# Kernel optimization log

Measured on AMD Instinct MI355X. Metric: run time of the kernel, lower is better.

The kernel has to match this reference:

```python
import jax, jax.numpy as jnp
import numpy as np

D_MODEL = 768
D_STATE = 16
D_CONV = 4
EXPAND = 2
N_LAYERS = 2
HEADDIM = 64
PATCH_DIM = 256
D_INNER = EXPAND * D_MODEL            # 1536
NHEADS = D_INNER // HEADDIM           # 24
CONV_DIM = D_INNER + 2 * D_STATE      # 1568 (x, B, C share the conv)
D_IN_PROJ = 2 * D_INNER + 2 * D_STATE + NHEADS  # 3128


def _mamba2(u, w_in, conv_w, conv_b, dt_bias, A_log, D, norm_w, w_out):
    """Mamba2 block (ngroups=1, rmsnorm=True, non-fused reference path)."""
    b, l, _ = u.shape
    zxbcdt = u @ w_in                                   # (b,l,D_IN_PROJ)
    z = zxbcdt[..., :D_INNER]
    xBC = zxbcdt[..., D_INNER:D_INNER + CONV_DIM]
    dt = jax.nn.softplus(zxbcdt[..., D_INNER + CONV_DIM:] + dt_bias)  # (b,l,H)
    # causal depthwise conv1d over L, then silu
    kernel = conv_w.T[:, None, :]                       # (D_CONV,1,CONV_DIM)
    xBC = jax.lax.conv_general_dilated(
        xBC, kernel, (1,), [(D_CONV - 1, 0)],
        dimension_numbers=('NLC', 'LIO', 'NLC'),
        feature_group_count=CONV_DIM) + conv_b
    xBC = jax.nn.silu(xBC)
    x = xBC[..., :D_INNER].reshape(b, l, NHEADS, HEADDIM)
    B = xBC[..., D_INNER:D_INNER + D_STATE]             # (b,l,N)
    C = xBC[..., D_INNER + D_STATE:]                    # (b,l,N)
    A = -jnp.exp(A_log)                                 # (H,)

    def step(h, inp):
        dt_t, x_t, b_t, c_t = inp                       # (b,H),(b,H,P),(b,N),(b,N)
        dA = jnp.exp(dt_t * A)                          # (b,H)
        h = h * dA[:, :, None, None] + jnp.einsum('bh,bhp,bn->bhpn', dt_t, x_t, b_t)
        y_t = jnp.einsum('bhpn,bn->bhp', h, c_t)
        return h, y_t

    h0 = jnp.zeros((b, NHEADS, HEADDIM, D_STATE), u.dtype)
    _, y = jax.lax.scan(step, h0,
                        (dt.swapaxes(0, 1), x.swapaxes(0, 1),
                         B.swapaxes(0, 1), C.swapaxes(0, 1)))
    y = y.swapaxes(0, 1) + x * D[:, None]               # skip: D per head
    y = y.reshape(b, l, D_INNER)
    # gated RMSNorm: rmsnorm(y * silu(z)) * weight
    g = y * jax.nn.silu(z)
    g = g * jax.lax.rsqrt(jnp.mean(g * g, axis=-1, keepdims=True) + 1e-5)
    y = g * norm_w
    return y @ w_out


def _backbone(patch_embeddings, Wp, bp, in_w, conv_w, conv_b, dt_bias,
              A_log, Dh, norm_w, out_w, bi_w, ls, fin_w):
    x = patch_embeddings @ Wp + bp
    for i in range(N_LAYERS):
        h_f = _mamba2(x, in_w[i, 0], conv_w[i, 0], conv_b[i, 0], dt_bias[i, 0],
                      A_log[i, 0], Dh[i, 0], norm_w[i, 0], out_w[i, 0])
        h_b = jnp.flip(_mamba2(jnp.flip(x, 1), in_w[i, 1], conv_w[i, 1],
                               conv_b[i, 1], dt_bias[i, 1], A_log[i, 1],
                               Dh[i, 1], norm_w[i, 1], out_w[i, 1]), 1)
        m = jnp.concatenate([h_f, h_b], axis=-1) @ bi_w[i]
        x = x + m * ls[i]
    # final RMSNorm with unit offset
    v = jnp.mean(x * x, axis=-1, keepdims=True)
    return x * jax.lax.rsqrt(v + 1e-6) * (1.0 + fin_w)


def setup_inputs() -> dict:
    key = jax.random.key(0)
    ks = jax.random.split(key, 14)
    L2 = (N_LAYERS, 2)
    pe = jax.random.normal(ks[0], (2, 2048, PATCH_DIM), jnp.float32)
    Wp = jax.random.normal(ks[1], (PATCH_DIM, D_MODEL), jnp.float32) * 0.02
    bp = jnp.zeros((D_MODEL,), jnp.float32)
    in_w = jax.random.normal(ks[2], L2 + (D_MODEL, D_IN_PROJ), jnp.float32) * 0.02
    conv_w = jax.random.normal(ks[3], L2 + (CONV_DIM, D_CONV), jnp.float32) * 0.2
    conv_b = jnp.zeros(L2 + (CONV_DIM,), jnp.float32)
    dt_bias = jax.random.uniform(ks[4], L2 + (NHEADS,), jnp.float32, -4.0, -2.0)
    A_log = jnp.log(jax.random.uniform(ks[5], L2 + (NHEADS,), jnp.float32, 1.0, 16.0))
    Dh = jax.random.normal(ks[6], L2 + (NHEADS,), jnp.float32) * 0.1 + 1.0
    norm_w = jnp.ones(L2 + (D_INNER,), jnp.float32)
    out_w = jax.random.normal(ks[7], L2 + (D_INNER, D_MODEL), jnp.float32) * 0.02
    bi_w = jax.random.normal(ks[8], (N_LAYERS, 2 * D_MODEL, D_MODEL), jnp.float32) * 0.02
    ls = jnp.full((N_LAYERS, D_MODEL), 1e-4, jnp.float32)
    fin_w = jnp.zeros((D_MODEL,), jnp.float32)
    return {"patch_embeddings": pe, "Wp": Wp, "bp": bp, "in_w": in_w,
            "conv_w": conv_w, "conv_b": conv_b, "dt_bias": dt_bias,
            "A_log": A_log, "Dh": Dh, "norm_w": norm_w, "out_w": out_w,
            "bi_w": bi_w, "ls": ls, "fin_w": fin_w}


def reference(patch_embeddings, Wp, bp, in_w, conv_w, conv_b, dt_bias,
              A_log, Dh, norm_w, out_w, bi_w, ls, fin_w):
    return _backbone(patch_embeddings, Wp, bp, in_w, conv_w, conv_b, dt_bias,
                     A_log, Dh, norm_w, out_w, bi_w, ls, fin_w)
```

## Files before the change

### kernel.cpp

```cpp
#include <hip/hip_runtime.h>

typedef unsigned short u16;
typedef short s16x8 __attribute__((ext_vector_type(8)));
typedef u16 u16x8 __attribute__((ext_vector_type(8)));
typedef float f32x4 __attribute__((ext_vector_type(4)));

__device__ inline float bf2f(u16 u) {
    union { unsigned int i; float f; } w; w.i = ((unsigned int)u) << 16; return w.f;
}
__device__ inline u16 f2bf(float f) {
    union { float f; unsigned int i; } w; w.f = f;
    unsigned int u = w.i;
    u += 0x7fffu + ((u >> 16) & 1u);
    return (u16)(u >> 16);
}

__global__ __launch_bounds__(256)
void wtransT(const float* __restrict__ src, u16* __restrict__ dst,
             int K, int N, int dstride, int src_z, int dz_hi, int dz_lo)
{
    int z = blockIdx.z;
    src += (size_t)z * src_z;
    dst += (size_t)(z >> 1) * dz_hi + (size_t)(z & 1) * dz_lo;
    __shared__ float t[32][33];
    int kt = blockIdx.y * 32, nt0 = blockIdx.x * 32;
    int lx = threadIdx.x & 31, ly = threadIdx.x >> 5;
#pragma unroll
    for (int i = 0; i < 32; i += 8) {
        int k = kt + ly + i, n = nt0 + lx;
        t[ly + i][lx] = (k < K && n < N) ? src[(size_t)k * N + n] : 0.f;
    }
    __syncthreads();
#pragma unroll
    for (int i = 0; i < 32; i += 8) {
        int n = nt0 + ly + i, k = kt + lx;
        if (n < N && k < K) dst[(size_t)n * dstride + k] = f2bf(t[lx][ly + i]);
    }
}

__global__ void cvtk(const float* __restrict__ src, u16* __restrict__ dst, int n) {
    int i = blockIdx.x * 256 + threadIdx.x;
    if (i < n) dst[i] = f2bf(src[i]);
}

__global__ __launch_bounds__(256, 2)
void gemm8(const u16* __restrict__ A, const u16* __restrict__ WT,
           int M, int N, int K,
           u16* __restrict__ bout, int ostride)
{
    __shared__ u16 lds8[2 * 16384];

    int mt, nt;
    {
        int nwg = gridDim.x * gridDim.y;
        int f = blockIdx.y * gridDim.x + blockIdx.x;
        int q = nwg >> 3, r = nwg & 7;
        int xcd = f & 7, lo = f >> 3;
        int wid = (xcd < r ? xcd * (q + 1) : r * (q + 1) + (xcd - r) * q) + lo;
        mt = wid % gridDim.y; nt = wid / gridDim.y;
    }

    const int tid  = threadIdx.x;
    const int lane = tid & 63;
    const int wave = tid >> 6;
    const int wm = wave >> 1, wn = wave & 1;
    const int r16 = lane & 15;
    const int lg  = lane >> 4;
    const int mb  = mt * 128;
    const int nb  = nt * 128;
    const int wbase = tid & 192;

    f32x4 acc[4][4];
#pragma unroll
    for (int mi = 0; mi < 4; mi++)
#pragma unroll
        for (int ni = 0; ni < 4; ni++)
            acc[mi][ni] = (f32x4){0.f, 0.f, 0.f, 0.f};

    auto stage = [&](int buf, int k0) {
        u16* bA = &lds8[buf * 16384];
        u16* bB = bA + 8192;
#pragma unroll
        for (int r = 0; r < 4; r++) {
            int e = r * 256 + tid;
            int row = e >> 3;
            int cbs = (e & 7) ^ (row & 7);
            const u16* g = A + (size_t)(mb + row) * K + k0 + cbs * 8;
            __builtin_amdgcn_global_load_lds(
                (const __attribute__((address_space(1))) void*)g,
                (__attribute__((address_space(3))) void*)&bA[(r * 256 + wbase) * 8],
                16, 0, 0);
        }
#pragma unroll
        for (int r = 0; r < 4; r++) {
            int e = r * 256 + tid;
            int row = e >> 3;
            int cbs = (e & 7) ^ (row & 7);
            const u16* g = WT + (size_t)(nb + row) * K + k0 + cbs * 8;
            __builtin_amdgcn_global_load_lds(
                (const __attribute__((address_space(1))) void*)g,
                (__attribute__((address_space(3))) void*)&bB[(r * 256 + wbase) * 8],
                16, 0, 0);
        }
    };

    const int ntk = K >> 6;
    stage(0, 0);
    stage(1, 64);
    asm volatile("s_waitcnt vmcnt(8)" ::: "memory");
    __builtin_amdgcn_sched_barrier(0);
    __builtin_amdgcn_s_barrier();

    for (int t = 0; t < ntk; t++) {
        const int buf = t & 1;
        const u16* bA = &lds8[buf * 16384];
        const u16* bB = bA + 8192;
        s16x8 a[4][2], b[4][2];
#pragma unroll
        for (int mf = 0; mf < 4; mf++)
#pragma unroll
            for (int kk = 0; kk < 2; kk++) {
                int row = wm * 64 + mf * 16 + r16;
                int cb = (kk * 4 + lg) ^ (row & 7);
                a[mf][kk] = *(const s16x8*)&bA[row * 64 + cb * 8];
            }
#pragma unroll
        for (int nf = 0; nf < 4; nf++)
#pragma unroll
            for (int kk = 0; kk < 2; kk++) {
                int row = wn * 64 + nf * 16 + r16;
                int cb = (kk * 4 + lg) ^ (row & 7);
                b[nf][kk] = *(const s16x8*)&bB[row * 64 + cb * 8];
            }
        asm volatile("s_waitcnt lgkmcnt(0)" ::: "memory");
        __builtin_amdgcn_sched_barrier(0);
        __builtin_amdgcn_s_barrier();
        if (t + 2 < ntk) {
            stage(buf, (t + 2) << 6);
            asm volatile("s_waitcnt vmcnt(8)" ::: "memory");
        } else {
            asm volatile("s_waitcnt vmcnt(0)" ::: "memory");
        }
        __builtin_amdgcn_sched_barrier(0);
        __builtin_amdgcn_s_barrier();
        __builtin_amdgcn_s_setprio(1);
#pragma unroll
        for (int mf = 0; mf < 4; mf++)
#pragma unroll
            for (int nf = 0; nf < 4; nf++) {
                acc[mf][nf] = __builtin_amdgcn_mfma_f32_16x16x32_bf16(
                    a[mf][0], b[nf][0], acc[mf][nf], 0, 0, 0);
                acc[mf][nf] = __builtin_amdgcn_mfma_f32_16x16x32_bf16(
                    a[mf][1], b[nf][1], acc[mf][nf], 0, 0, 0);
            }
        __builtin_amdgcn_s_setprio(0);
    }

#pragma unroll
    for (int mf = 0; mf < 4; mf++) {
        const int rowb = mb + wm * 64 + mf * 16 + lg * 4;
#pragma unroll
        for (int nf = 0; nf < 4; nf++) {
            int col = nb + wn * 64 + nf * 16 + r16;
            if (col < N) {
#pragma unroll
                for (int j = 0; j < 4; j++)
                    bout[(size_t)(rowb + j) * ostride + col] = f2bf(acc[mf][nf][j]);
            }
        }
    }
}

__global__ __launch_bounds__(256, 2)
void gemm9(const u16* __restrict__ A, const u16* __restrict__ WT, int K,
           float* __restrict__ fout, u16* __restrict__ bout,
           const float* __restrict__ lsv)
{
    __shared__ u16 lds9[2 * 12288];

    int mt, nt;
    {
        int nwg = gridDim.x * gridDim.y;
        int f = blockIdx.y * gridDim.x + blockIdx.x;
        int q = nwg >> 3, r = nwg & 7;
        int xcd = f & 7, lo = f >> 3;
        int wid = (xcd < r ? xcd * (q + 1) : r * (q + 1) + (xcd - r) * q) + lo;
        mt = wid % gridDim.y; nt = wid / gridDim.y;
    }

    const int tid  = threadIdx.x;
    const int lane = tid & 63;
    const int wave = tid >> 6;
    const int wm = wave >> 1, wn = wave & 1;
    const int r16 = lane & 15;
    const int lg  = lane >> 4;
    const int mb  = mt * 128;
    const int nb  = nt * 64;
    const int wbase = tid & 192;

    f32x4 acc[4][2];
#pragma unroll
    for (int mi = 0; mi < 4; mi++)
#pragma unroll
        for (int ni = 0; ni < 2; ni++)
            acc[mi][ni] = (f32x4){0.f, 0.f, 0.f, 0.f};

    auto stage = [&](int buf, int k0) {
        u16* bA = &lds9[buf * 12288];
#pragma unroll
        for (int rr = 0; rr < 6; rr++) {
            int e = rr * 256 + tid;
            int row = e >> 3;
            int cbs = (e & 7) ^ (row & 7);
            const u16* g = (rr < 4)
                ? A  + (size_t)(mb + row) * K + k0 + cbs * 8
                : WT + (size_t)(nb + row - 128) * K + k0 + cbs * 8;
            __builtin_amdgcn_global_load_lds(
                (const __attribute__((address_space(1))) void*)g,
                (__attribute__((address_space(3))) void*)&bA[(rr * 256 + wbase) * 8],
                16, 0, 0);
        }
    };

    const int ntk = K >> 6;
    stage(0, 0);
    stage(1, 64);
    asm volatile("s_waitcnt vmcnt(6)" ::: "memory");
    __builtin_amdgcn_sched_barrier(0);
    __builtin_amdgcn_s_barrier();

    for (int t = 0; t < ntk; t++) {
        const int buf = t & 1;
        const u16* bA = &lds9[buf * 12288];
        const u16* bB = bA + 8192;
        s16x8 a[4][2], b[2][2];
#pragma unroll
        for (int mf = 0; mf < 4; mf++)
#pragma unroll
            for (int kk = 0; kk < 2; kk++) {
                int row = wm * 64 + mf * 16 + r16;
                int cb = (kk * 4 + lg) ^ (row & 7);
                a[mf][kk] = *(const s16x8*)&bA[row * 64 + cb * 8];
            }
#pragma unroll
        for (int nf = 0; nf < 2; nf++)
#pragma unroll
            for (int kk = 0; kk < 2; kk++) {
                int row = wn * 32 + nf * 16 + r16;
                int cb = (kk * 4 + lg) ^ (row & 7);
                b[nf][kk] = *(const s16x8*)&bB[row * 64 + cb * 8];
            }
        asm volatile("s_waitcnt lgkmcnt(0)" ::: "memory");
        __builtin_amdgcn_sched_barrier(0);
        __builtin_amdgcn_s_barrier();
        if (t + 2 < ntk) {
            stage(buf, (t + 2) << 6);
            asm volatile("s_waitcnt vmcnt(6)" ::: "memory");
        } else {
            asm volatile("s_waitcnt vmcnt(0)" ::: "memory");
        }
        __builtin_amdgcn_sched_barrier(0);
        __builtin_amdgcn_s_barrier();
        __builtin_amdgcn_s_setprio(1);
#pragma unroll
        for (int mf = 0; mf < 4; mf++)
#pragma unroll
            for (int nf = 0; nf < 2; nf++) {
                acc[mf][nf] = __builtin_amdgcn_mfma_f32_16x16x32_bf16(
                    a[mf][0], b[nf][0], acc[mf][nf], 0, 0, 0);
                acc[mf][nf] = __builtin_amdgcn_mfma_f32_16x16x32_bf16(
                    a[mf][1], b[nf][1], acc[mf][nf], 0, 0, 0);
            }
        __builtin_amdgcn_s_setprio(0);
    }

#pragma unroll
    for (int mf = 0; mf < 4; mf++) {
        const int rowb = mb + wm * 64 + mf * 16 + lg * 4;
#pragma unroll
        for (int nf = 0; nf < 2; nf++) {
            int col = nb + wn * 32 + nf * 16 + r16;
#pragma unroll
            for (int j = 0; j < 4; j++) {
                size_t o = (size_t)(rowb + j) * 768 + col;
                float xv = fout[o] + acc[mf][nf][j] * lsv[col];
                fout[o] = xv; bout[o] = f2bf(xv);
            }
        }
    }
}

__global__ __launch_bounds__(256, 2)
void gemm10(const u16* __restrict__ A, const u16* __restrict__ WT, int K,
            u16* __restrict__ bout, int ostride,
            size_t aZ, size_t wZ, size_t oZ, int ocolZ)
{
    __shared__ u16 ldsA[2 * 12288];

    {
        int z = blockIdx.z;
        A += (size_t)z * aZ; WT += (size_t)z * wZ;
        bout += (size_t)(z >> 1) * oZ + (size_t)(z & 1) * ocolZ;
    }
    int mt, nt;
    {
        int nwg = gridDim.x * gridDim.y;
        int f = blockIdx.y * gridDim.x + blockIdx.x;
        int q = nwg >> 3, r = nwg & 7;
        int xcd = f & 7, lo = f >> 3;
        int wid = (xcd < r ? xcd * (q + 1) : r * (q + 1) + (xcd - r) * q) + lo;
        mt = wid % gridDim.y; nt = wid / gridDim.y;
    }

    const int tid  = threadIdx.x;
    const int lane = tid & 63;
    const int wave = tid >> 6;
    const int wm = wave >> 1, wn = wave & 1;
    const int r16 = lane & 15;
    const int lg  = lane >> 4;
    const int mb  = mt * 128;
    const int nb  = nt * 64;
    const int wbase = tid & 192;

    f32x4 acc[4][2];
#pragma unroll
    for (int mi = 0; mi < 4; mi++)
#pragma unroll
        for (int ni = 0; ni < 2; ni++)
            acc[mi][ni] = (f32x4){0.f, 0.f, 0.f, 0.f};

    auto stage = [&](int buf, int k0) {
        u16* bA = &ldsA[buf * 12288];
#pragma unroll
        for (int rr = 0; rr < 6; rr++) {
            int e = rr * 256 + tid;
            int row = e >> 3;
            int cbs = (e & 7) ^ (row & 7);
            const u16* g = (rr < 4)
                ? A  + (size_t)(mb + row) * K + k0 + cbs * 8
                : WT + (size_t)(nb + row - 128) * K + k0 + cbs * 8;
            __builtin_amdgcn_global_load_lds(
                (const __attribute__((address_space(1))) void*)g,
                (__attribute__((address_space(3))) void*)&bA[(rr * 256 + wbase) * 8],
                16, 0, 0);
        }
    };

    const int ntk = K >> 6;
    stage(0, 0);
    stage(1, 64);
    asm volatile("s_waitcnt vmcnt(6)" ::: "memory");
    __builtin_amdgcn_sched_barrier(0);
    __builtin_amdgcn_s_barrier();

    for (int t = 0; t < ntk; t++) {
        const int buf = t & 1;
        const u16* bA = &ldsA[buf * 12288];
        const u16* bB = bA + 8192;
        s16x8 a[4][2], b[2][2];
#pragma unroll
        for (int mf = 0; mf < 4; mf++)
#pragma unroll
            for (int kk = 0; kk < 2; kk++) {
                int row = wm * 64 + mf * 16 + r16;
                int cb = (kk * 4 + lg) ^ (row & 7);
                a[mf][kk] = *(const s16x8*)&bA[row * 64 + cb * 8];
            }
#pragma unroll
        for (int nf = 0; nf < 2; nf++)
#pragma unroll
            for (int kk = 0; kk < 2; kk++) {
                int row = wn * 32 + nf * 16 + r16;
                int cb = (kk * 4 + lg) ^ (row & 7);
                b[nf][kk] = *(const s16x8*)&bB[row * 64 + cb * 8];
            }
        asm volatile("s_waitcnt lgkmcnt(0)" ::: "memory");
        __builtin_amdgcn_sched_barrier(0);
        __builtin_amdgcn_s_barrier();
        if (t + 2 < ntk) {
            stage(buf, (t + 2) << 6);
            asm volatile("s_waitcnt vmcnt(6)" ::: "memory");
        } else {
            asm volatile("s_waitcnt vmcnt(0)" ::: "memory");
        }
        __builtin_amdgcn_sched_barrier(0);
        __builtin_amdgcn_s_barrier();
        __builtin_amdgcn_s_setprio(1);
#pragma unroll
        for (int mf = 0; mf < 4; mf++)
#pragma unroll
            for (int nf = 0; nf < 2; nf++) {
                acc[mf][nf] = __builtin_amdgcn_mfma_f32_16x16x32_bf16(
                    a[mf][0], b[nf][0], acc[mf][nf], 0, 0, 0);
                acc[mf][nf] = __builtin_amdgcn_mfma_f32_16x16x32_bf16(
                    a[mf][1], b[nf][1], acc[mf][nf], 0, 0, 0);
            }
        __builtin_amdgcn_s_setprio(0);
    }

#pragma unroll
    for (int mf = 0; mf < 4; mf++) {
        const int rowb = mb + wm * 64 + mf * 16 + lg * 4;
#pragma unroll
        for (int nf = 0; nf < 2; nf++) {
            int col = nb + wn * 32 + nf * 16 + r16;
#pragma unroll
            for (int j = 0; j < 4; j++)
                bout[(size_t)(rowb + j) * ostride + col] = f2bf(acc[mf][nf][j]);
        }
    }
}

__global__ __launch_bounds__(256, 2)
void gemm11(const u16* __restrict__ A, const u16* __restrict__ WT, int K,
            float* __restrict__ fout, u16* __restrict__ bout,
            const float* __restrict__ bias)
{
    __shared__ u16 ldsB[2 * 12288];

    int mt, nt;
    {
        int nwg = gridDim.x * gridDim.y;
        int f = blockIdx.y * gridDim.x + blockIdx.x;
        int q = nwg >> 3, r = nwg & 7;
        int xcd = f & 7, lo = f >> 3;
        int wid = (xcd < r ? xcd * (q + 1) : r * (q + 1) + (xcd - r) * q) + lo;
        mt = wid % gridDim.y; nt = wid / gridDim.y;
    }

    const int tid  = threadIdx.x;
    const int lane = tid & 63;
    const int wave = tid >> 6;
    const int wm = wave >> 1, wn = wave & 1;
    const int r16 = lane & 15;
    const int lg  = lane >> 4;
    const int mb  = mt * 128;
    const int nb  = nt * 64;
    const int wbase = tid & 192;

    f32x4 acc[4][2];
#pragma unroll
    for (int mi = 0; mi < 4; mi++)
#pragma unroll
        for (int ni = 0; ni < 2; ni++)
            acc[mi][ni] = (f32x4){0.f, 0.f, 0.f, 0.f};

    auto stage = [&](int buf, int k0) {
        u16* bA = &ldsB[buf * 12288];
#pragma unroll
        for (int rr = 0; rr < 6; rr++) {
            int e = rr * 256 + tid;
            int row = e >> 3;
            int cbs = (e & 7) ^ (row & 7);
            const u16* g = (rr < 4)
                ? A  + (size_t)(mb + row) * K + k0 + cbs * 8
                : WT + (size_t)(nb + row - 128) * K + k0 + cbs * 8;
            __builtin_amdgcn_global_load_lds(
                (const __attribute__((address_space(1))) void*)g,
                (__attribute__((address_space(3))) void*)&bA[(rr * 256 + wbase) * 8],
                16, 0, 0);
        }
    };

    const int ntk = K >> 6;
    stage(0, 0);
    stage(1, 64);
    asm volatile("s_waitcnt vmcnt(6)" ::: "memory");
    __builtin_amdgcn_sched_barrier(0);
    __builtin_amdgcn_s_barrier();

    for (int t = 0; t < ntk; t++) {
        const int buf = t & 1;
        const u16* bA = &ldsB[buf * 12288];
        const u16* bB = bA + 8192;
        s16x8 a[4][2], b[2][2];
#pragma unroll
        for (int mf = 0; mf < 4; mf++)
#pragma unroll
            for (int kk = 0; kk < 2; kk++) {
                int row = wm * 64 + mf * 16 + r16;
                int cb = (kk * 4 + lg) ^ (row & 7);
                a[mf][kk] = *(const s16x8*)&bA[row * 64 + cb * 8];
            }
#pragma unroll
        for (int nf = 0; nf < 2; nf++)
#pragma unroll
            for (int kk = 0; kk < 2; kk++) {
                int row = wn * 32 + nf * 16 + r16;
                int cb = (kk * 4 + lg) ^ (row & 7);
                b[nf][kk] = *(const s16x8*)&bB[row * 64 + cb * 8];
            }
        asm volatile("s_waitcnt lgkmcnt(0)" ::: "memory");
        __builtin_amdgcn_sched_barrier(0);
        __builtin_amdgcn_s_barrier();
        if (t + 2 < ntk) {
            stage(buf, (t + 2) << 6);
            asm volatile("s_waitcnt vmcnt(6)" ::: "memory");
        } else {
            asm volatile("s_waitcnt vmcnt(0)" ::: "memory");
        }
        __builtin_amdgcn_sched_barrier(0);
        __builtin_amdgcn_s_barrier();
        __builtin_amdgcn_s_setprio(1);
#pragma unroll
        for (int mf = 0; mf < 4; mf++)
#pragma unroll
            for (int nf = 0; nf < 2; nf++) {
                acc[mf][nf] = __builtin_amdgcn_mfma_f32_16x16x32_bf16(
                    a[mf][0], b[nf][0], acc[mf][nf], 0, 0, 0);
                acc[mf][nf] = __builtin_amdgcn_mfma_f32_16x16x32_bf16(
                    a[mf][1], b[nf][1], acc[mf][nf], 0, 0, 0);
            }
        __builtin_amdgcn_s_setprio(0);
    }

#pragma unroll
    for (int mf = 0; mf < 4; mf++) {
        const int rowb = mb + wm * 64 + mf * 16 + lg * 4;
#pragma unroll
        for (int nf = 0; nf < 2; nf++) {
            int col = nb + wn * 32 + nf * 16 + r16;
#pragma unroll
            for (int j = 0; j < 4; j++) {
                float v = acc[mf][nf][j] + bias[col];
                size_t o = (size_t)(rowb + j) * 768 + col;
                fout[o] = v; bout[o] = f2bf(v);
            }
        }
    }
}

__global__ void preK(const u16* __restrict__ zxAll, float* __restrict__ dtAll,
                     u16* __restrict__ bcAll, const float* __restrict__ dtb,
                     const float* __restrict__ cw, const float* __restrict__ cb)
{
    int idx = blockIdx.x * 256 + threadIdx.x;
    if (idx < 2 * 4096 * 24) {
        int dir = idx / (4096 * 24);
        int r   = idx % (4096 * 24);
        int row = r / 24, h = r % 24;
        float raw = bf2f(zxAll[(size_t)row * 6256 + dir * 3128 + 3104 + h]) + dtb[dir * 24 + h];
        dtAll[((size_t)dir * 4096 + row) * 24 + h] = raw > 20.f ? raw : log1pf(__expf(raw));
        return;
    }
    int v = idx - 2 * 4096 * 24;
    if (v >= 2 * 4096 * 32) return;
    int ch  = v & 31;
    int row = (v >> 5) & 4095;
    int dir = v >> 17;
    int l   = row & 2047;
    int chg = 1536 + ch;
    float acc = cb[dir * 1568 + chg];
    const float* w = cw + ((size_t)dir * 1568 + chg) * 4;
#pragma unroll
    for (int k = 0; k < 4; k++) {
        int ll = dir ? (l + 3 - k) : (l - 3 + k);
        if (ll >= 0 && ll < 2048)
            acc += bf2f(zxAll[(size_t)(row + (ll - l)) * 6256 + dir * 3128 + chg]) * w[k];
    }
    acc = acc / (1.f + __expf(-acc));
    bcAll[((size_t)dir * 4096 + row) * 32 + ch] = f2bf(acc);
}

__global__ __launch_bounds__(256)
void scan1k(const u16* __restrict__ zxAll, const float* __restrict__ dtAll,
            const u16* __restrict__ bcAll,
            const float* __restrict__ cw, const float* __restrict__ cb,
            const float* __restrict__ Alog, const float* __restrict__ Dhp,
            u16* __restrict__ yAll, float* __restrict__ states, float* __restrict__ decays)
{
    const int c   = blockIdx.x;
    const int bh  = blockIdx.y;
    const int dir = blockIdx.z;
    const int b = bh / 24, h = bh % 24;
    const float* dtp = dtAll + (size_t)dir * 4096 * 24;
    const u16* bcp = bcAll + (size_t)dir * 4096 * 32;
    u16* yp = yAll + dir * 1536;
    const float Av = -__expf(Alog[dir * 24 + h]);
    const float Dv = Dhp[dir * 24 + h];
    const int inst = (dir * 2 + b) * 24 + h;

    const int tid  = threadIdx.x;
    const int lane = tid & 63;
    const int wave = tid >> 6;
    const int r16  = lane & 15;
    const int ks   = (lane >> 4) * 8;

    __shared__ u16 xT[64][72];
    __shared__ u16 Gs[64][72];
    __shared__ u16 Bs[64][40];
    __shared__ u16 Cs[64][40];
    __shared__ u16 SBT[16][72];
    __shared__ float dts[64], cds[64];

    const u16* zxd = zxAll + dir * 3128 + 1536;
    auto growp = [&](int ii) -> const u16* {
        int l = dir ? (2047 - ii) : ii;
        return zxd + ((size_t)b * 2048 + l) * 6256;
    };
    auto rowof = [&](int t) -> size_t {
        int i = c * 64 + t;
        int l = dir ? (2047 - i) : i;
        return (size_t)b * 2048 + l;
    };
    const u16x8 zz = {0,0,0,0,0,0,0,0};

    {
        int tr = tid >> 2, pg = tid & 3;
        int chb = h * 64 + pg * 16;
        int i0 = c * 64 + tr;
        u16x8 tv[4][2];
#pragma unroll
        for (int k = 0; k < 4; k++) {
            int ii = i0 - 3 + k;
            if (ii >= 0) {
                const u16* s = growp(ii) + chb;
                tv[k][0] = *(const u16x8*)s;
                tv[k][1] = *(const u16x8*)(s + 8);
            } else { tv[k][0] = zz; tv[k][1] = zz; }
        }
        const float* cwp = cw + ((size_t)dir * 1568 + chb) * 4;
        const float* cbp = cb + (size_t)dir * 1568 + chb;
#pragma unroll
        for (int j = 0; j < 16; j++) {
            f32x4 wj = *(const f32x4*)(cwp + j * 4);
            float a = cbp[j];
            int hi = j >> 3, lo2 = j & 7;
            a += bf2f(tv[0][hi][lo2]) * wj[0] + bf2f(tv[1][hi][lo2]) * wj[1]
               + bf2f(tv[2][hi][lo2]) * wj[2] + bf2f(tv[3][hi][lo2]) * wj[3];
            a = a / (1.f + __expf(-a));
            xT[pg * 16 + j][tr] = f2bf(a);
        }
    }
    {
        int t = tid & 63, which = tid >> 6;
        if (which < 2) {
            const u16* src = bcp + rowof(t) * 32 + which * 16;
            u16* dst = which ? &Cs[t][0] : &Bs[t][0];
            *(u16x8*)dst = *(const u16x8*)src;
            *(u16x8*)(dst + 8) = *(const u16x8*)(src + 8);
        } else {
            u16* dst = (which == 2) ? &Bs[t][16] : &Cs[t][16];
            *(u16x8*)dst = zz; *(u16x8*)(dst + 8) = zz;
        }
    }
    if (tid < 64) {
        float v = dtp[rowof(tid) * 24 + h];
        dts[tid] = v;
        float s = v;
#pragma unroll
        for (int o = 1; o < 64; o <<= 1) {
            float nvl = __shfl_up(s, o, 64);
            if (lane >= o) s += nvl;
        }
        cds[tid] = s;
    }
    __syncthreads();

    {
        const s16x8 af = *(const s16x8*)&Cs[wave * 16 + r16][ks];
#pragma unroll
        for (int st = 0; st < 4; st++) {
            const s16x8 bfr = *(const s16x8*)&Bs[st * 16 + r16][ks];
            f32x4 a2 = {0.f, 0.f, 0.f, 0.f};
            a2 = __builtin_amdgcn_mfma_f32_16x16x32_bf16(af, bfr, a2, 0, 0, 0);
            int s = st * 16 + (lane & 15);
            int tbase = wave * 16 + (lane >> 4) * 4;
            float cs = cds[s], dtv = dts[s];
#pragma unroll
            for (int j = 0; j < 4; j++) {
                int t = tbase + j;
                float g = 0.f;
                if (s <= t) {
                    g = a2[j] * dtv * __expf(Av * (cds[t] - cs));
                    if (s == t) g += Dv;
                }
                Gs[t][s] = f2bf(g);
            }
        }
    }
    {
        float cdT = cds[63];
        int s = tid & 63;
        float sc = __expf(Av * (cdT - cds[s])) * dts[s];
#pragma unroll
        for (int it = 0; it < 4; it++) {
            int n = (tid >> 6) + it * 4;
            SBT[n][s] = f2bf(sc * bf2f(Bs[s][n]));
        }
    }
    __syncthreads();

    {
#pragma unroll
        for (int pt = 0; pt < 4; pt++) {
            f32x4 a2 = {0.f, 0.f, 0.f, 0.f};
#pragma unroll
            for (int kk = 0; kk < 2; kk++) {
                s16x8 af = *(const s16x8*)&Gs[wave * 16 + r16][kk * 32 + ks];
                s16x8 bfr = *(const s16x8*)&xT[pt * 16 + r16][kk * 32 + ks];
                a2 = __builtin_amdgcn_mfma_f32_16x16x32_bf16(af, bfr, a2, 0, 0, 0);
            }
            int p = pt * 16 + (lane & 15);
            int tbase = wave * 16 + (lane >> 4) * 4;
#pragma unroll
            for (int j = 0; j < 4; j++) {
                size_t row = rowof(tbase + j);
                yp[row * 3072 + h * 64 + p] = f2bf(a2[j]);
            }
        }
    }
    {
        f32x4 a2 = {0.f, 0.f, 0.f, 0.f};
#pragma unroll
        for (int kk = 0; kk < 2; kk++) {
            s16x8 af = *(const s16x8*)&xT[wave * 16 + r16][kk * 32 + ks];
            s16x8 bfr = *(const s16x8*)&SBT[r16][kk * 32 + ks];
            a2 = __builtin_amdgcn_mfma_f32_16x16x32_bf16(af, bfr, a2, 0, 0, 0);
        }
        int n = lane & 15;
        int pbase = wave * 16 + (lane >> 4) * 4;
        float* st = states + ((size_t)inst * 32 + c) * 1024;
#pragma unroll
        for (int j = 0; j < 4; j++) st[(pbase + j) * 16 + n] = a2[j];
        if (tid == 0) decays[inst * 32 + c] = __expf(Av * cds[63]);
    }
}

__global__ __launch_bounds__(256)
void scan2k(float* __restrict__ states, const float* __restrict__ decays)
{
    int inst = blockIdx.x;
    int tid = threadIdx.x;
    float* base = states + (size_t)inst * 32 * 1024 + tid * 4;
    const float* dec = decays + inst * 32;
    f32x4 hreg = {0.f, 0.f, 0.f, 0.f};
    f32x4 L = *(f32x4*)base;
    for (int cc = 0; cc < 32; cc++) {
        f32x4 Lnext;
        if (cc + 1 < 32) Lnext = *(f32x4*)(base + (cc + 1) * 1024);
        *(f32x4*)(base + cc * 1024) = hreg;
        float d = dec[cc];
        hreg = hreg * d + L;
        L = Lnext;
    }
}

__global__ __launch_bounds__(256)
void scan3k(const float* __restrict__ states,
            const u16* __restrict__ bcAll, const float* __restrict__ dtAll,
            const float* __restrict__ Alog, u16* __restrict__ yAll)
{
    const int c   = blockIdx.x + 1;
    const int bh  = blockIdx.y;
    const int dir = blockIdx.z;
    const int b = bh / 24, h = bh % 24;
    const float* dtp = dtAll + (size_t)dir * 4096 * 24;
    const u16* bcp = bcAll + (size_t)dir * 4096 * 32;
    u16* yp = yAll + dir * 1536;
    const float Av = -__expf(Alog[dir * 24 + h]);
    const int inst = (dir * 2 + b) * 24 + h;
    const int tid = threadIdx.x;

    __shared__ float hs[64][20];
    __shared__ u16 Cs3[64][16];
    __shared__ float ets[64];

    auto rowof = [&](int t) -> size_t {
        int i = c * 64 + t;
        int l = dir ? (2047 - i) : i;
        return (size_t)b * 2048 + l;
    };

    {
        const float* sp = states + ((size_t)inst * 32 + c) * 1024 + tid * 4;
        f32x4 v = *(const f32x4*)sp;
        int e = tid * 4;
        int p = e >> 4, n = e & 15;
        hs[p][n] = v[0]; hs[p][n+1] = v[1]; hs[p][n+2] = v[2]; hs[p][n+3] = v[3];
    }
    if (tid < 64) {
        size_t row = rowof(tid);
        const u16* src = bcp + row * 32 + 16;
        *(u16x8*)&Cs3[tid][0] = *(const u16x8*)src;
        *(u16x8*)&Cs3[tid][8] = *(const u16x8*)(src + 8);
        float v = dtp[row * 24 + h];
        float s = v;
#pragma unroll
        for (int o = 1; o < 64; o <<= 1) {
            float nvl = __shfl_up(s, o, 64);
            if ((tid & 63) >= o) s += nvl;
        }
        ets[tid] = __expf(Av * s);
    }
    __syncthreads();

    int t = tid >> 2, pg = tid & 3;
    float cv[16];
    float et = ets[t];
#pragma unroll
    for (int n = 0; n < 16; n++) cv[n] = bf2f(Cs3[t][n]) * et;
    size_t row = rowof(t);
    u16* yrow = yp + row * 3072 + h * 64 + pg * 16;
    u16x8 ya = *(u16x8*)yrow;
    u16x8 yb = *(u16x8*)(yrow + 8);
#pragma unroll
    for (int jj = 0; jj < 16; jj++) {
        int p = pg * 16 + jj;
        float acc = 0.f;
#pragma unroll
        for (int q = 0; q < 4; q++) {
            f32x4 hv = *(const f32x4*)&hs[p][q * 4];
            acc += cv[q*4]*hv[0] + cv[q*4+1]*hv[1] + cv[q*4+2]*hv[2] + cv[q*4+3]*hv[3];
        }
        if (jj < 8) ya[jj] = f2bf(bf2f(ya[jj]) + acc);
        else        yb[jj - 8] = f2bf(bf2f(yb[jj - 8]) + acc);
    }
    *(u16x8*)yrow = ya;
    *(u16x8*)(yrow + 8) = yb;
}

__global__ __launch_bounds__(256)
void gatek(const u16* __restrict__ zxAll, u16* __restrict__ yAll,
           const float* __restrict__ nw)
{
    int row = blockIdx.x, dir = blockIdx.y;
    const u16* zx = zxAll + (size_t)row * 6256 + dir * 3128;
    u16* y = yAll + (size_t)row * 3072 + dir * 1536;
    const float* nwp = nw + dir * 1536;
    int tid = threadIdx.x;
    float g[6]; float s = 0.f;
#pragma unroll
    for (int j = 0; j < 6; j++) {
        int c = j * 256 + tid;
        float z  = bf2f(zx[c]);
        float yv = bf2f(y[c]);
        float gv = yv * z / (1.f + __expf(-z));
        g[j] = gv; s += gv * gv;
    }
    __shared__ float red[4];
    for (int o = 32; o; o >>= 1) s += __shfl_down(s, o, 64);
    if ((tid & 63) == 0) red[tid >> 6] = s;
    __syncthreads();
    s = red[0] + red[1] + red[2] + red[3];
    float sc = rsqrtf(s * (1.f / 1536.f) + 1e-5f);
#pragma unroll
    for (int j = 0; j < 6; j++) {
        int c = j * 256 + tid;
        y[c] = f2bf(g[j] * sc * nwp[c]);
    }
}

__global__ __launch_bounds__(256)
void finalk(const float* __restrict__ x, const float* __restrict__ fw, float* __restrict__ out)
{
    int row = blockIdx.x; int tid = threadIdx.x;
    const float* xr = x + (size_t)row * 768;
    float v[3]; float s = 0.f;
#pragma unroll
    for (int j = 0; j < 3; j++) {
        int c = j * 256 + tid;
        v[j] = xr[c]; s += v[j] * v[j];
    }
    __shared__ float red[4];
    for (int o = 32; o; o >>= 1) s += __shfl_down(s, o, 64);
    if ((tid & 63) == 0) red[tid >> 6] = s;
    __syncthreads();
    s = red[0] + red[1] + red[2] + red[3];
    float sc = rsqrtf(s * (1.f / 768.f) + 1e-6f);
#pragma unroll
    for (int j = 0; j < 3; j++) {
        int c = j * 256 + tid;
        out[(size_t)row * 768 + c] = v[j] * sc * (1.f + fw[c]);
    }
}

extern "C" void kernel_launch(void* const* d_in, const int* in_sizes, int n_in,
                              void* d_out, int out_size, void* d_ws, size_t ws_size,
                              hipStream_t stream)
{
    const float* pe      = (const float*)d_in[0];
    const float* Wp      = (const float*)d_in[1];
    const float* bp      = (const float*)d_in[2];
    const float* in_w    = (const float*)d_in[3];
    const float* conv_w  = (const float*)d_in[4];
    const float* conv_b  = (const float*)d_in[5];
    const float* dt_bias = (const float*)d_in[6];
    const float* A_log   = (const float*)d_in[7];
    const float* Dh      = (const float*)d_in[8];
    const float* norm_w  = (const float*)d_in[9];
    const float* out_w   = (const float*)d_in[10];
    const float* bi_w    = (const float*)d_in[11];
    const float* ls      = (const float*)d_in[12];
    const float* fin_w   = (const float*)d_in[13];

    char* wp = (char*)d_ws;
    auto alloc = [&](size_t bytes) {
        char* r = wp; wp += (bytes + 255) & ~(size_t)255; return r;
    };
    u16*   WpT    = (u16*)  alloc((size_t)768 * 256 * 2);
    u16*   inWT   = (u16*)  alloc((size_t)2 * 6272 * 768 * 2);
    u16*   outWB  = (u16*)  alloc((size_t)4 * 1536 * 768 * 2);
    u16*   biWT   = (u16*)  alloc((size_t)4 * 768 * 768 * 2);
    u16*   WcombT = (u16*)  alloc((size_t)2 * 768 * 3072 * 2);
    u16*   peB    = (u16*)  alloc((size_t)4096 * 256 * 2);
    float* x      = (float*)alloc((size_t)4096 * 768 * 4);
    u16*   xb     = (u16*)  alloc((size_t)4096 * 768 * 2);
    u16*   zxAll  = (u16*)  alloc((size_t)4096 * 6256 * 2);
    float* dtAll  = (float*)alloc((size_t)2 * 4096 * 24 * 4);
    u16*   bcAll  = (u16*)  alloc((size_t)2 * 4096 * 32 * 2);
    u16*   yAll   = (u16*)  alloc((size_t)4096 * 3072 * 2);
    float* states = (float*)alloc((size_t)96 * 32 * 1024 * 4);
    float* decays = (float*)alloc((size_t)96 * 32 * 4);

    wtransT<<<dim3(24, 8, 1), 256, 0, stream>>>(Wp, WpT, 256, 768, 256, 0, 0, 0);
    wtransT<<<dim3(98, 24, 4), 256, 0, stream>>>(in_w, inWT, 768, 3128, 768,
                                                 2402304, 4816896, 2402304);
    wtransT<<<dim3(24, 24, 4), 256, 0, stream>>>(bi_w, biWT, 768, 768, 768,
                                                 589824, 1179648, 589824);
    cvtk<<<(4 * 1536 * 768 + 255) / 256, 256, 0, stream>>>(out_w, outWB, 4 * 1536 * 768);
    cvtk<<<4096, 256, 0, stream>>>(pe, peB, 4096 * 256);

    gemm10<<<dim3(24, 6, 4), 256, 0, stream>>>(
        biWT, outWB, 768, WcombT, 3072,
        (size_t)589824, (size_t)1179648, (size_t)768 * 3072, 1536);

    gemm11<<<dim3(12, 32), 256, 0, stream>>>(peB, WpT, 256, x, xb, bp);

    for (int i = 0; i < 2; i++) {
        gemm8<<<dim3(49, 32, 1), 256, 0, stream>>>(
            xb, inWT + (size_t)i * 6272 * 768, 4096, 6256, 768, zxAll, 6256);
        preK<<<(2 * 4096 * 56 + 255) / 256, 256, 0, stream>>>(
            zxAll, dtAll, bcAll, dt_bias + i * 48,
            conv_w + (size_t)i * 2 * 1568 * 4, conv_b + (size_t)i * 2 * 1568);
        scan1k<<<dim3(32, 48, 2), 256, 0, stream>>>(zxAll, dtAll, bcAll,
                                                    conv_w + (size_t)i * 2 * 1568 * 4,
                                                    conv_b + (size_t)i * 2 * 1568,
                                                    A_log + i * 48, Dh + i * 48,
                                                    yAll, states, decays);
        scan2k<<<96, 256, 0, stream>>>(states, decays);
        scan3k<<<dim3(31, 48, 2), 256, 0, stream>>>(states, bcAll, dtAll,
                                                    A_log + i * 48, yAll);
        gatek<<<dim3(4096, 2), 256, 0, stream>>>(zxAll, yAll, norm_w + (size_t)i * 2 * 1536);
        gemm9<<<dim3(12, 32, 1), 256, 0, stream>>>(
            yAll, WcombT + (size_t)i * 768 * 3072, 3072, x, xb, ls + i * 768);
    }

    finalk<<<4096, 256, 0, stream>>>(x, fin_w, (float*)d_out);
}
```

Measured before the change: 475.2 us.

## Replace in-projection GEMM with 256x256-tile 8-wave kernel and interleaved staging

The in-projection GEMM moves from 128x128 tiles with 4 waves to 256x256 tiles with 8 waves, using 128KB of dynamic LDS. Global-to-LDS loads for the next K-step are spread across four MFMA phases, each split by barriers, so loads overlap compute. The larger tile raises arithmetic intensity and reuse of A and B. The weight buffer is padded to 6400 rows so the last N tile stays in bounds. The cost is one workgroup per CU, heavy register use, and a coarser grid of 400 tiles, which can leave the tail of the wave unbalanced.

```diff
diff --git a/kernel.cpp b/kernel.cpp
--- a/kernel.cpp
+++ b/kernel.cpp
@@ -43,12 +43,12 @@
     if (i < n) dst[i] = f2bf(src[i]);
 }
 
-__global__ __launch_bounds__(256, 2)
-void gemm8(const u16* __restrict__ A, const u16* __restrict__ WT,
-           int M, int N, int K,
+__global__ __launch_bounds__(512, 1)
+void gemmY(const u16* __restrict__ A, const u16* __restrict__ WT,
+           int N, int K,
            u16* __restrict__ bout, int ostride)
 {
-    __shared__ u16 lds8[2 * 16384];
+    extern __shared__ u16 ldsY[];
 
     int mt, nt;
     {
@@ -62,110 +62,176 @@
 
     const int tid  = threadIdx.x;
     const int lane = tid & 63;
-    const int wave = tid >> 6;
-    const int wm = wave >> 1, wn = wave & 1;
-    const int r16 = lane & 15;
-    const int lg  = lane >> 4;
-    const int mb  = mt * 128;
-    const int nb  = nt * 128;
-    const int wbase = tid & 192;
-
-    f32x4 acc[4][4];
-#pragma unroll
-    for (int mi = 0; mi < 4; mi++)
-#pragma unroll
-        for (int ni = 0; ni < 4; ni++)
-            acc[mi][ni] = (f32x4){0.f, 0.f, 0.f, 0.f};
-
-    auto stage = [&](int buf, int k0) {
-        u16* bA = &lds8[buf * 16384];
-        u16* bB = bA + 8192;
-#pragma unroll
-        for (int r = 0; r < 4; r++) {
-            int e = r * 256 + tid;
-            int row = e >> 3;
-            int cbs = (e & 7) ^ (row & 7);
-            const u16* g = A + (size_t)(mb + row) * K + k0 + cbs * 8;
-            __builtin_amdgcn_global_load_lds(
-                (const __attribute__((address_space(1))) void*)g,
-                (__attribute__((address_space(3))) void*)&bA[(r * 256 + wbase) * 8],
-                16, 0, 0);
-        }
-#pragma unroll
-        for (int r = 0; r < 4; r++) {
-            int e = r * 256 + tid;
-            int row = e >> 3;
-            int cbs = (e & 7) ^ (row & 7);
-            const u16* g = WT + (size_t)(nb + row) * K + k0 + cbs * 8;
-            __builtin_amdgcn_global_load_lds(
-                (const __attribute__((address_space(1))) void*)g,
-                (__attribute__((address_space(3))) void*)&bB[(r * 256 + wbase) * 8],
-                16, 0, 0);
-        }
+    const int wv   = tid >> 6;
+    const int wm   = wv >> 2;
+    const int wn   = wv & 3;
+    const int r16  = lane & 15;
+    const int lg   = lane >> 4;
+    const int mb   = mt * 256;
+    const int nb   = nt * 256;
+
+    f32x4 acc[8][4];
+#pragma unroll
+    for (int i = 0; i < 8; i++)
+#pragma unroll
+        for (int c = 0; c < 4; c++)
+            acc[i][c] = (f32x4){0.f, 0.f, 0.f, 0.f};
+
+    auto stageAq = [&](int buf, int k0, int q) {
+        int lr = tid >> 3, c8 = tid & 7;
+        int row = (lr < 32) ? (q * 32 + lr) : (128 + q * 32 + (lr - 32));
+        int cbs = c8 ^ (row & 7);
+        const u16* g = A + (size_t)(mb + row) * K + k0 + cbs * 8;
+        int dstelem = buf * 32768 +
+            ((wv < 4) ? (q * 2048 + wv * 512) : (8192 + q * 2048 + (wv - 4) * 512));
+        __builtin_amdgcn_global_load_lds(
+            (const __attribute__((address_space(1))) void*)g,
+            (__attribute__((address_space(3))) void*)&ldsY[dstelem], 16, 0, 0);
     };
+    auto stageBq = [&](int buf, int k0, int bq) {
+        int row = bq * 64 + (tid >> 3), c8 = tid & 7;
+        int cbs = c8 ^ (row & 7);
+        const u16* g = WT + (size_t)(nb + row) * K + k0 + cbs * 8;
+        int dstelem = buf * 32768 + 16384 + bq * 4096 + wv * 512;
+        __builtin_amdgcn_global_load_lds(
+            (const __attribute__((address_space(1))) void*)g,
+            (__attribute__((address_space(3))) void*)&ldsY[dstelem], 16, 0, 0);
+    };
 
     const int ntk = K >> 6;
-    stage(0, 0);
-    stage(1, 64);
-    asm volatile("s_waitcnt vmcnt(8)" ::: "memory");
-    __builtin_amdgcn_sched_barrier(0);
-    __builtin_amdgcn_s_barrier();
+#pragma unroll
+    for (int q = 0; q < 4; q++) stageAq(0, 0, q);
+#pragma unroll
+    for (int q = 0; q < 4; q++) stageBq(0, 0, q);
+    stageAq(1, 64, 0); stageAq(1, 64, 1); stageAq(1, 64, 2);
+#pragma unroll
+    for (int q = 0; q < 4; q++) stageBq(1, 64, q);
+
+    s16x8 b[4][2], aA[2][2], aB[2][2];
 
     for (int t = 0; t < ntk; t++) {
         const int buf = t & 1;
-        const u16* bA = &lds8[buf * 16384];
-        const u16* bB = bA + 8192;
-        s16x8 a[4][2], b[4][2];
-#pragma unroll
-        for (int mf = 0; mf < 4; mf++)
-#pragma unroll
-            for (int kk = 0; kk < 2; kk++) {
-                int row = wm * 64 + mf * 16 + r16;
-                int cb = (kk * 4 + lg) ^ (row & 7);
-                a[mf][kk] = *(const s16x8*)&bA[row * 64 + cb * 8];
-            }
-#pragma unroll
-        for (int nf = 0; nf < 4; nf++)
-#pragma unroll
-            for (int kk = 0; kk < 2; kk++) {
-                int row = wn * 64 + nf * 16 + r16;
-                int cb = (kk * 4 + lg) ^ (row & 7);
-                b[nf][kk] = *(const s16x8*)&bB[row * 64 + cb * 8];
-            }
+        const int bA0 = buf * 32768;
+        const int bB0 = buf * 32768 + 16384;
+        const int k1 = (t + 1) << 6;
+        const int k2 = (t + 2) << 6;
+
+        asm volatile("s_waitcnt vmcnt(7)" ::: "memory");
+        __builtin_amdgcn_sched_barrier(0);
+        __builtin_amdgcn_s_barrier();
+        __builtin_amdgcn_sched_barrier(0);
+        stageAq(buf ^ 1, k1, 3);
+#pragma unroll
+        for (int c = 0; c < 4; c++)
+#pragma unroll
+            for (int kk = 0; kk < 2; kk++) {
+                int row = wn * 64 + c * 16 + r16;
+                b[c][kk] = *(const s16x8*)&ldsY[bB0 + row * 64 + ((kk * 4 + lg) ^ (row & 7)) * 8];
+            }
+#pragma unroll
+        for (int i = 0; i < 2; i++)
+#pragma unroll
+            for (int kk = 0; kk < 2; kk++) {
+                int row = wm * 128 + i * 16 + r16;
+                aA[i][kk] = *(const s16x8*)&ldsY[bA0 + row * 64 + ((kk * 4 + lg) ^ (row & 7)) * 8];
+            }
+#pragma unroll
+        for (int i = 0; i < 2; i++)
+#pragma unroll
+            for (int kk = 0; kk < 2; kk++) {
+                int row = wm * 128 + (2 + i) * 16 + r16;
+                aB[i][kk] = *(const s16x8*)&ldsY[bA0 + row * 64 + ((kk * 4 + lg) ^ (row & 7)) * 8];
+            }
+        __builtin_amdgcn_sched_barrier(0);
+        asm volatile("s_waitcnt lgkmcnt(4)" ::: "memory");
+        __builtin_amdgcn_sched_barrier(0);
+        __builtin_amdgcn_s_setprio(1);
+#pragma unroll
+        for (int i = 0; i < 2; i++)
+#pragma unroll
+            for (int c = 0; c < 4; c++) {
+                acc[i][c] = __builtin_amdgcn_mfma_f32_16x16x32_bf16(aA[i][0], b[c][0], acc[i][c], 0, 0, 0);
+                acc[i][c] = __builtin_amdgcn_mfma_f32_16x16x32_bf16(aA[i][1], b[c][1], acc[i][c], 0, 0, 0);
+            }
+        __builtin_amdgcn_s_setprio(0);
+
+        __builtin_amdgcn_sched_barrier(0);
+        __builtin_amdgcn_s_barrier();
+        __builtin_amdgcn_sched_barrier(0);
+        stageAq(buf, k2, 0); stageBq(buf, k2, 0); stageBq(buf, k2, 1);
+#pragma unroll
+        for (int i = 0; i < 2; i++)
+#pragma unroll
+            for (int kk = 0; kk < 2; kk++) {
+                int row = wm * 128 + (4 + i) * 16 + r16;
+                aA[i][kk] = *(const s16x8*)&ldsY[bA0 + row * 64 + ((kk * 4 + lg) ^ (row & 7)) * 8];
+            }
+        __builtin_amdgcn_sched_barrier(0);
+        asm volatile("s_waitcnt lgkmcnt(4)" ::: "memory");
+        __builtin_amdgcn_sched_barrier(0);
+        __builtin_amdgcn_s_setprio(1);
+#pragma unroll
+        for (int i = 0; i < 2; i++)
+#pragma unroll
+            for (int c = 0; c < 4; c++) {
+                acc[2 + i][c] = __builtin_amdgcn_mfma_f32_16x16x32_bf16(aB[i][0], b[c][0], acc[2 + i][c], 0, 0, 0);
+                acc[2 + i][c] = __builtin_amdgcn_mfma_f32_16x16x32_bf16(aB[i][1], b[c][1], acc[2 + i][c], 0, 0, 0);
+            }
+        __builtin_amdgcn_s_setprio(0);
+
+        __builtin_amdgcn_sched_barrier(0);
+        __builtin_amdgcn_s_barrier();
+        __builtin_amdgcn_sched_barrier(0);
+        stageAq(buf, k2, 1); stageBq(buf, k2, 2);
+#pragma unroll
+        for (int i = 0; i < 2; i++)
+#pragma unroll
+            for (int kk = 0; kk < 2; kk++) {
+                int row = wm * 128 + (6 + i) * 16 + r16;
+                aB[i][kk] = *(const s16x8*)&ldsY[bA0 + row * 64 + ((kk * 4 + lg) ^ (row & 7)) * 8];
+            }
+        __builtin_amdgcn_sched_barrier(0);
+        asm volatile("s_waitcnt lgkmcnt(4)" ::: "memory");
+        __builtin_amdgcn_sched_barrier(0);
+        __builtin_amdgcn_s_setprio(1);
+#pragma unroll
+        for (int i = 0; i < 2; i++)
+#pragma unroll
+            for (int c = 0; c < 4; c++) {
+                acc[4 + i][c] = __builtin_amdgcn_mfma_f32_16x16x32_bf16(aA[i][0], b[c][0], acc[4 + i][c], 0, 0, 0);
+                acc[4 + i][c] = __builtin_amdgcn_mfma_f32_16x16x32_bf16(aA[i][1], b[c][1], acc[4 + i][c], 0, 0, 0);
+            }
+        __builtin_amdgcn_s_setprio(0);
+
+        __builtin_amdgcn_sched_barrier(0);
+        __builtin_amdgcn_s_barrier();
+        __builtin_amdgcn_sched_barrier(0);
+        stageAq(buf, k2, 2); stageBq(buf, k2, 3);
+        __builtin_amdgcn_sched_barrier(0);
         asm volatile("s_waitcnt lgkmcnt(0)" ::: "memory");
         __builtin_amdgcn_sched_barrier(0);
-        __builtin_amdgcn_s_barrier();
-        if (t + 2 < ntk) {
-            stage(buf, (t + 2) << 6);
-            asm volatile("s_waitcnt vmcnt(8)" ::: "memory");
-        } else {
-            asm volatile("s_waitcnt vmcnt(0)" ::: "memory");
-        }
-        __builtin_amdgcn_sched_barrier(0);
-        __builtin_amdgcn_s_barrier();
         __builtin_amdgcn_s_setprio(1);
 #pragma unroll
-        for (int mf = 0; mf < 4; mf++)
-#pragma unroll
-            for (int nf = 0; nf < 4; nf++) {
-                acc[mf][nf] = __builtin_amdgcn_mfma_f32_16x16x32_bf16(
-                    a[mf][0], b[nf][0], acc[mf][nf], 0, 0, 0);
-                acc[mf][nf] = __builtin_amdgcn_mfma_f32_16x16x32_bf16(
-                    a[mf][1], b[nf][1], acc[mf][nf], 0, 0, 0);
+        for (int i = 0; i < 2; i++)
+#pragma unroll
+            for (int c = 0; c < 4; c++) {
+                acc[6 + i][c] = __builtin_amdgcn_mfma_f32_16x16x32_bf16(aB[i][0], b[c][0], acc[6 + i][c], 0, 0, 0);
+                acc[6 + i][c] = __builtin_amdgcn_mfma_f32_16x16x32_bf16(aB[i][1], b[c][1], acc[6 + i][c], 0, 0, 0);
             }
         __builtin_amdgcn_s_setprio(0);
-    }
-
-#pragma unroll
-    for (int mf = 0; mf < 4; mf++) {
-        const int rowb = mb + wm * 64 + mf * 16 + lg * 4;
-#pragma unroll
-        for (int nf = 0; nf < 4; nf++) {
-            int col = nb + wn * 64 + nf * 16 + r16;
+        __builtin_amdgcn_sched_barrier(0);
+    }
+
+#pragma unroll
+    for (int fr = 0; fr < 8; fr++) {
+        const int rowb = mb + wm * 128 + fr * 16 + lg * 4;
+#pragma unroll
+        for (int c = 0; c < 4; c++) {
+            int col = nb + wn * 64 + c * 16 + r16;
             if (col < N) {
 #pragma unroll
                 for (int j = 0; j < 4; j++)
-                    bout[(size_t)(rowb + j) * ostride + col] = f2bf(acc[mf][nf][j]);
+                    bout[(size_t)(rowb + j) * ostride + col] = f2bf(acc[fr][c][j]);
             }
         }
     }
@@ -899,7 +965,7 @@
         char* r = wp; wp += (bytes + 255) & ~(size_t)255; return r;
     };
     u16*   WpT    = (u16*)  alloc((size_t)768 * 256 * 2);
-    u16*   inWT   = (u16*)  alloc((size_t)2 * 6272 * 768 * 2);
+    u16*   inWT   = (u16*)  alloc(((size_t)2 * 6400 * 768 + 4096) * 2);
     u16*   outWB  = (u16*)  alloc((size_t)4 * 1536 * 768 * 2);
     u16*   biWT   = (u16*)  alloc((size_t)4 * 768 * 768 * 2);
     u16*   WcombT = (u16*)  alloc((size_t)2 * 768 * 3072 * 2);
@@ -915,7 +981,7 @@
 
     wtransT<<<dim3(24, 8, 1), 256, 0, stream>>>(Wp, WpT, 256, 768, 256, 0, 0, 0);
     wtransT<<<dim3(98, 24, 4), 256, 0, stream>>>(in_w, inWT, 768, 3128, 768,
-                                                 2402304, 4816896, 2402304);
+                                                 2402304, 4915200, 2402304);
     wtransT<<<dim3(24, 24, 4), 256, 0, stream>>>(bi_w, biWT, 768, 768, 768,
                                                  589824, 1179648, 589824);
     cvtk<<<(4 * 1536 * 768 + 255) / 256, 256, 0, stream>>>(out_w, outWB, 4 * 1536 * 768);
@@ -927,9 +993,12 @@
 
     gemm11<<<dim3(12, 32), 256, 0, stream>>>(peB, WpT, 256, x, xb, bp);
 
+    hipFuncSetAttribute((const void*)gemmY,
+                        hipFuncAttributeMaxDynamicSharedMemorySize, 131072);
+
     for (int i = 0; i < 2; i++) {
-        gemm8<<<dim3(49, 32, 1), 256, 0, stream>>>(
-            xb, inWT + (size_t)i * 6272 * 768, 4096, 6256, 768, zxAll, 6256);
+        gemmY<<<dim3(25, 16), 512, 131072, stream>>>(
+            xb, inWT + (size_t)i * 6400 * 768, 6256, 768, zxAll, 6256);
         preK<<<(2 * 4096 * 56 + 255) / 256, 256, 0, stream>>>(
             zxAll, dtAll, bcAll, dt_bias + i * 48,
             conv_w + (size_t)i * 2 * 1568 * 4, conv_b + (size_t)i * 2 * 1568);
```

Result: faster. 454.9 us (-4.3%).
